# Performance work log

Hardware: AMD Instinct MI355X
Metric: run time of the kernel (lower is better)

## Reference

```python
import jax, jax.numpy as jnp
import numpy as np

H2 = 128  # 2*hidden_dim

def setup_inputs() -> dict:
    key = jax.random.key(0)
    k1, k2, k3 = jax.random.split(key, 3)
    B, Lb, Lp = 64, 1024, 1024
    body = jax.random.normal(k1, (B, Lb, H2), dtype=jnp.float32)
    pun = jax.random.normal(k2, (B, Lp, H2), dtype=jnp.float32)
    w_u = jax.random.normal(k3, (3 * H2, 1), dtype=jnp.float32)
    return {"batch_size": B, "body": body, "pun": pun, "w_u": w_u}

def reference(batch_size, body, pun, w_u):
    # score[b,i,j] = [body_i ; pun_j ; body_i*pun_j] @ w_u
    # Decompose w_u into the three 128-dim blocks so the double loop fuses
    # into two matvecs plus one weighted batched GEMM.
    w = w_u[:, 0]
    w1, w2, w3 = w[:H2], w[H2:2 * H2], w[2 * H2:]
    s_body = jnp.einsum('bid,d->bi', body, w1)          # [B, Lb]
    s_pun = jnp.einsum('bjd,d->bj', pun, w2)            # [B, Lp]
    s_cross = jnp.einsum('bid,bjd->bij', body * w3, pun)  # [B, Lb, Lp]
    return s_cross + s_body[:, :, None] + s_pun[:, None, :]
```

## Files before the change

kernel.cpp:

```cpp
#include <hip/hip_runtime.h>


#define LSEQ 1024
#define H2K  128


typedef __attribute__((ext_vector_type(8))) short bfrag;
typedef __attribute__((ext_vector_type(4))) float f32x4;

__device__ __forceinline__ short f2bf(float x) {
    unsigned u = __float_as_uint(x);
    unsigned r = (u + 0x7fff + ((u >> 16) & 1)) >> 16;
    return (short)r;
}
__device__ __forceinline__ float bf2f(short s) {
    return __uint_as_float(((unsigned)(unsigned short)s) << 16);
}

__device__ __forceinline__ void ld16(void* lds, const void* g) {
    __builtin_amdgcn_global_load_lds(
        (const __attribute__((address_space(1))) void*)g,
        (__attribute__((address_space(3))) void*)lds, 16, 0, 0);
}

__global__ __launch_bounds__(256) void prep_kernel(
    const float* __restrict__ body, const float* __restrict__ pun,
    const float* __restrict__ w_u, float* __restrict__ ws)
{
    const int flag = blockIdx.y;
    const int lane = threadIdx.x & 63;
    const int wv   = threadIdx.x >> 6;
    const size_t row = (size_t)blockIdx.x * 4 + wv;

    const float* src = (flag ? pun : body) + row * H2K;
    const float2 v  = *(const float2*)(src + lane * 2);
    const float2 wm = *(const float2*)(w_u + flag * H2K + lane * 2);

    float p = v.x * wm.x + v.y * wm.y;
    p += __shfl_xor(p, 32);
    p += __shfl_xor(p, 16);
    p += __shfl_xor(p, 8);
    p += __shfl_xor(p, 4);
    p += __shfl_xor(p, 2);
    p += __shfl_xor(p, 1);
    if (lane == 0) ws[(size_t)flag * 65536 + row] = p;

    float cx = v.x, cy = v.y;
    if (!flag) {
        const float2 w3v = *(const float2*)(w_u + 2 * H2K + lane * 2);
        cx *= w3v.x; cy *= w3v.y;
    }
    const short h0 = f2bf(cx), h1 = f2bf(cy);
    const short l0 = f2bf(cx - bf2f(h0)), l1 = f2bf(cy - bf2f(h1));

    short* hb = (short*)(ws + 131072) + (size_t)flag * 16777216 + row * H2K + lane * 2;
    *(unsigned*)hb =
        ((unsigned)(unsigned short)h0) | ((unsigned)(unsigned short)h1 << 16);
    *(unsigned*)(hb + 8388608) =
        ((unsigned)(unsigned short)l0) | ((unsigned)(unsigned short)l1 << 16);
}

__global__ __launch_bounds__(512, 2) void align_mfma(
    const float* __restrict__ ws, float* __restrict__ out)
{
    __shared__ __align__(16) short Ch[2][8192], Cl[2][8192];
    __shared__ __align__(16) short Ph[2][8192], Pl[2][8192];

    const int nwg = gridDim.x;
    const int bid = blockIdx.x;
    const int tid = (bid & 7) * (nwg >> 3) + (bid >> 3);
    const int bb = tid >> 4;
    const int ti = ((tid >> 2) & 3) * 256;
    const int tj = (tid & 3) * 256;

    const int t    = threadIdx.x;
    const int lane = t & 63;
    const int w    = t >> 6;

    const int srow = w * 16 + (lane & 15);
    const int k8   = lane >> 4;
    const short* base = (const short*)(ws + 131072);
    const size_t crow = (size_t)(bb * LSEQ + ti + srow) * H2K + k8 * 8;
    const size_t prow = (size_t)(bb * LSEQ + tj + srow) * H2K + k8 * 8;
    const short* gCh = base + crow;
    const short* gCl = base + 8388608 + crow;
    const short* gPh = base + 16777216 + prow;
    const short* gPl = base + 25165824 + prow;
    const size_t R2 = (size_t)128 * H2K;

#define STAGE(u, c) do {                                         \
        ld16(&Ch[u][t * 8],         gCh + (c) * 32);             \
        ld16(&Ch[u][(512 + t) * 8], gCh + R2 + (c) * 32);        \
        ld16(&Cl[u][t * 8],         gCl + (c) * 32);             \
        ld16(&Cl[u][(512 + t) * 8], gCl + R2 + (c) * 32);        \
        ld16(&Ph[u][t * 8],         gPh + (c) * 32);             \
        ld16(&Ph[u][(512 + t) * 8], gPh + R2 + (c) * 32);        \
        ld16(&Pl[u][t * 8],         gPl + (c) * 32);             \
        ld16(&Pl[u][(512 + t) * 8], gPl + R2 + (c) * 32);        \
    } while (0)

    const int jg = w & 1;
    const int ig = w >> 1;
    f32x4 acc[8][4] = {};

    STAGE(0, 0);

#pragma unroll
    for (int kt = 0; kt < 4; ++kt) {
        const int cur = kt & 1, nxt = cur ^ 1;

        if (kt < 3) STAGE(nxt, kt + 1);
        __builtin_amdgcn_sched_barrier(0);
        if (kt < 3) asm volatile("s_waitcnt vmcnt(8)" ::: "memory");
        else        asm volatile("s_waitcnt vmcnt(0)" ::: "memory");
        __builtin_amdgcn_s_barrier();

        bfrag ph[8], pl[8];
#pragma unroll
        for (int jj = 0; jj < 8; ++jj) {
            ph[jj] = *(const bfrag*)&Ph[cur][((jg * 8 + jj) * 64 + lane) * 8];
            pl[jj] = *(const bfrag*)&Pl[cur][((jg * 8 + jj) * 64 + lane) * 8];
        }
#pragma unroll
        for (int ii = 0; ii < 4; ++ii) {
            const bfrag ch = *(const bfrag*)&Ch[cur][((ig * 4 + ii) * 64 + lane) * 8];
            const bfrag cl = *(const bfrag*)&Cl[cur][((ig * 4 + ii) * 64 + lane) * 8];
#pragma unroll
            for (int jj = 0; jj < 8; ++jj) {
                acc[jj][ii] = __builtin_amdgcn_mfma_f32_16x16x32_bf16(ph[jj], ch, acc[jj][ii], 0, 0, 0);
                acc[jj][ii] = __builtin_amdgcn_mfma_f32_16x16x32_bf16(ph[jj], cl, acc[jj][ii], 0, 0, 0);
                acc[jj][ii] = __builtin_amdgcn_mfma_f32_16x16x32_bf16(pl[jj], ch, acc[jj][ii], 0, 0, 0);
            }
        }

        if (kt < 3) __builtin_amdgcn_s_barrier();
        __builtin_amdgcn_sched_barrier(0);
    }
#undef STAGE

    const float* sbp = ws + (size_t)bb * LSEQ;
    const float* spp = ws + 65536 + (size_t)bb * LSEQ;
    const int qd = lane >> 4, ln = lane & 15;
#pragma unroll
    for (int jj = 0; jj < 8; ++jj) {
        const int j0 = tj + (jg * 8 + jj) * 16 + qd * 4;
        const float4 spv = *(const float4*)(spp + j0);
#pragma unroll
        for (int ii = 0; ii < 4; ++ii) {
            const int row = ti + (ig * 4 + ii) * 16 + ln;
            const float sb = sbp[row];
            const f32x4 a = acc[jj][ii];
            float4 r = { a[0] + sb + spv.x, a[1] + sb + spv.y,
                         a[2] + sb + spv.z, a[3] + sb + spv.w };
            *(float4*)&out[((size_t)bb * LSEQ + row) * LSEQ + j0] = r;
        }
    }
}

extern "C" void kernel_launch(void* const* d_in, const int* in_sizes, int n_in,
                              void* d_out, int out_size, void* d_ws, size_t ws_size,
                              hipStream_t stream) {
    const float* body = (const float*)d_in[1];
    const float* pun  = (const float*)d_in[2];
    const float* w_u  = (const float*)d_in[3];
    float* out = (float*)d_out;
    float* ws  = (float*)d_ws;
    const int B = in_sizes[1] / (LSEQ * H2K);

    dim3 g1((B * LSEQ) / 4, 2, 1);
    prep_kernel<<<g1, 256, 0, stream>>>(body, pun, w_u, ws);

    dim3 g2(B * 16, 1, 1);
    align_mfma<<<g2, 512, 0, stream>>>(ws, out);
}
```

Baseline: 410.6 us.

## Shrink MFMA tile to 128x256, drop double buffering, raise occupancy

Halves the per-workgroup output tile from 256x256 to 128x256, doubling the grid. It removes LDS double buffering in favour of single-buffered staging with __syncthreads, and halves the per-wave accumulators. Launch bounds go from 2 to 4 workgroups per CU, so latency is hidden by occupancy rather than by software pipelining. The cost is less operand reuse per tile, more redundant loads of the pun rows, and exposed load latency within each workgroup.

```diff
diff --git a/kernel.cpp b/kernel.cpp
--- a/kernel.cpp
+++ b/kernel.cpp
@@ -60,18 +60,19 @@
         ((unsigned)(unsigned short)l0) | ((unsigned)(unsigned short)l1 << 16);
 }
 
-__global__ __launch_bounds__(512, 2) void align_mfma(
+__global__ __launch_bounds__(512, 4) void align_mfma(
     const float* __restrict__ ws, float* __restrict__ out)
 {
-    __shared__ __align__(16) short Ch[2][8192], Cl[2][8192];
-    __shared__ __align__(16) short Ph[2][8192], Pl[2][8192];
+    __shared__ __align__(16) short Ch[4096], Cl[4096];
+    __shared__ __align__(16) short Ph[8192], Pl[8192];
 
     const int nwg = gridDim.x;
     const int bid = blockIdx.x;
     const int tid = (bid & 7) * (nwg >> 3) + (bid >> 3);
-    const int bb = tid >> 4;
-    const int ti = ((tid >> 2) & 3) * 256;
-    const int tj = (tid & 3) * 256;
+    const int bb = tid >> 5;
+    const int r5 = tid & 31;
+    const int ti = (r5 >> 2) * 128;
+    const int tj = (r5 & 3) * 256;
 
     const int t    = threadIdx.x;
     const int lane = t & 63;
@@ -86,64 +87,48 @@
     const short* gCl = base + 8388608 + crow;
     const short* gPh = base + 16777216 + prow;
     const short* gPl = base + 25165824 + prow;
-    const size_t R2 = (size_t)128 * H2K;
+    const size_t R2OFF = (size_t)128 * H2K;
 
-#define STAGE(u, c) do {                                         \
-        ld16(&Ch[u][t * 8],         gCh + (c) * 32);             \
-        ld16(&Ch[u][(512 + t) * 8], gCh + R2 + (c) * 32);        \
-        ld16(&Cl[u][t * 8],         gCl + (c) * 32);             \
-        ld16(&Cl[u][(512 + t) * 8], gCl + R2 + (c) * 32);        \
-        ld16(&Ph[u][t * 8],         gPh + (c) * 32);             \
-        ld16(&Ph[u][(512 + t) * 8], gPh + R2 + (c) * 32);        \
-        ld16(&Pl[u][t * 8],         gPl + (c) * 32);             \
-        ld16(&Pl[u][(512 + t) * 8], gPl + R2 + (c) * 32);        \
-    } while (0)
+    const int jg = w & 3;
+    const int ig = w >> 2;
+    f32x4 acc[4][4] = {};
 
-    const int jg = w & 1;
-    const int ig = w >> 1;
-    f32x4 acc[8][4] = {};
+    for (int kt = 0; kt < 4; ++kt) {
+        if (kt) __syncthreads();
 
-    STAGE(0, 0);
+        ld16(&Ch[t * 8],         gCh + kt * 32);
+        ld16(&Cl[t * 8],         gCl + kt * 32);
+        ld16(&Ph[t * 8],         gPh + kt * 32);
+        ld16(&Ph[(512 + t) * 8], gPh + R2OFF + kt * 32);
+        ld16(&Pl[t * 8],         gPl + kt * 32);
+        ld16(&Pl[(512 + t) * 8], gPl + R2OFF + kt * 32);
+        __syncthreads();
 
+        bfrag ph[4], pl[4];
 #pragma unroll
-    for (int kt = 0; kt < 4; ++kt) {
-        const int cur = kt & 1, nxt = cur ^ 1;
-
-        if (kt < 3) STAGE(nxt, kt + 1);
-        __builtin_amdgcn_sched_barrier(0);
-        if (kt < 3) asm volatile("s_waitcnt vmcnt(8)" ::: "memory");
-        else        asm volatile("s_waitcnt vmcnt(0)" ::: "memory");
-        __builtin_amdgcn_s_barrier();
-
-        bfrag ph[8], pl[8];
-#pragma unroll
-        for (int jj = 0; jj < 8; ++jj) {
-            ph[jj] = *(const bfrag*)&Ph[cur][((jg * 8 + jj) * 64 + lane) * 8];
-            pl[jj] = *(const bfrag*)&Pl[cur][((jg * 8 + jj) * 64 + lane) * 8];
+        for (int jj = 0; jj < 4; ++jj) {
+            ph[jj] = *(const bfrag*)&Ph[((jg * 4 + jj) * 64 + lane) * 8];
+            pl[jj] = *(const bfrag*)&Pl[((jg * 4 + jj) * 64 + lane) * 8];
         }
 #pragma unroll
         for (int ii = 0; ii < 4; ++ii) {
-            const bfrag ch = *(const bfrag*)&Ch[cur][((ig * 4 + ii) * 64 + lane) * 8];
-            const bfrag cl = *(const bfrag*)&Cl[cur][((ig * 4 + ii) * 64 + lane) * 8];
+            const bfrag ch = *(const bfrag*)&Ch[((ig * 4 + ii) * 64 + lane) * 8];
+            const bfrag cl = *(const bfrag*)&Cl[((ig * 4 + ii) * 64 + lane) * 8];
 #pragma unroll
-            for (int jj = 0; jj < 8; ++jj) {
+            for (int jj = 0; jj < 4; ++jj) {
                 acc[jj][ii] = __builtin_amdgcn_mfma_f32_16x16x32_bf16(ph[jj], ch, acc[jj][ii], 0, 0, 0);
                 acc[jj][ii] = __builtin_amdgcn_mfma_f32_16x16x32_bf16(ph[jj], cl, acc[jj][ii], 0, 0, 0);
                 acc[jj][ii] = __builtin_amdgcn_mfma_f32_16x16x32_bf16(pl[jj], ch, acc[jj][ii], 0, 0, 0);
             }
         }
-
-        if (kt < 3) __builtin_amdgcn_s_barrier();
-        __builtin_amdgcn_sched_barrier(0);
     }
-#undef STAGE
 
     const float* sbp = ws + (size_t)bb * LSEQ;
     const float* spp = ws + 65536 + (size_t)bb * LSEQ;
     const int qd = lane >> 4, ln = lane & 15;
 #pragma unroll
-    for (int jj = 0; jj < 8; ++jj) {
-        const int j0 = tj + (jg * 8 + jj) * 16 + qd * 4;
+    for (int jj = 0; jj < 4; ++jj) {
+        const int j0 = tj + (jg * 4 + jj) * 16 + qd * 4;
         const float4 spv = *(const float4*)(spp + j0);
 #pragma unroll
         for (int ii = 0; ii < 4; ++ii) {
@@ -170,6 +155,6 @@
     dim3 g1((B * LSEQ) / 4, 2, 1);
     prep_kernel<<<g1, 256, 0, stream>>>(body, pun, w_u, ws);
 
-    dim3 g2(B * 16, 1, 1);
+    dim3 g2(B * 32, 1, 1);
     align_mfma<<<g2, 512, 0, stream>>>(ws, out);
 }
```

Measured after the change: 427.0 us. 1.04x slower.
